# Kernel tuning notes

Hardware: AMD Instinct MI355X
Metric: run time of the kernel (lower is better)

## Reference

```python
import jax, jax.numpy as jnp
import numpy as np

PAST = 16
FUTURE = 4
DIM = 64
INPUT_SIZE = 256
NUM_LAYERS = 3
DILATION = [1, 2, 4, 8]
INPUT_LENGTH = 1024
BATCH = 16
NEG_INF = -1e9


def _dilated_masks(length, num_layers, dilation):
    # mask[i, t, s] == True means position t may NOT attend to position s in layer i.
    # Layer i attends to s = t - k*dilation[i] for k in [0, window) with
    # window = dilation[i+1] // dilation[i] (causal, dilated local window).
    idx = np.arange(length)
    diff = idx[:, None] - idx[None, :]  # t - s
    masks = []
    for i in range(num_layers):
        d = dilation[i]
        window = dilation[i + 1] // d
        allowed = (diff >= 0) & (diff % d == 0) & (diff < window * d)
        masks.append(~allowed)
    return jnp.asarray(np.stack(masks, 0))


def setup_inputs() -> dict:
    key = jax.random.key(0)
    k_inp, k_w, k_b = jax.random.split(key, 3)
    inp = jax.random.normal(k_inp, (BATCH, INPUT_LENGTH, INPUT_SIZE), dtype=jnp.float32)
    # BottleLinear(input_size, output_size): plain Linear over last dim
    out_size = FUTURE * DIM
    bound = 1.0 / np.sqrt(INPUT_SIZE)
    W_out = jax.random.uniform(k_w, (out_size, INPUT_SIZE), minval=-bound, maxval=bound, dtype=jnp.float32)
    b_out = jax.random.uniform(k_b, (out_size,), minval=-bound, maxval=bound, dtype=jnp.float32)
    masks = _dilated_masks(INPUT_LENGTH, NUM_LAYERS, DILATION)
    return {"inp": inp, "W_out": W_out, "b_out": b_out, "masks": masks}


def reference(inp, W_out, b_out, masks):
    # inp: [B, L, D]; masks: [num_layers, L, L] bool (True = masked)
    B, L, D = inp.shape
    scale = 1.0 / jnp.sqrt(jnp.asarray(D, inp.dtype))
    residual = inp[:, PAST:, :DIM][:, :, None, :]  # [B, L-past, 1, dim]
    out = inp
    attns = []
    for i in range(NUM_LAYERS):
        mask = masks[i, :L, :L]
        scores = jnp.einsum('bld,bmd->blm', out, out) * scale
        scores = jnp.where(mask[None], NEG_INF, scores)
        attn = jax.nn.softmax(scores, axis=-1)  # [B, L, L]
        # dropout=0.0 (eval); residual self-attention layer
        out = jnp.einsum('blm,bmd->bld', attn, out) + out
        attns.append(attn)
    o = out[:, PAST:]  # [B, L-past, D]
    o = jnp.einsum('bld,od->blo', o, W_out) + b_out
    o = o.reshape(B, L - PAST, FUTURE, DIM) + residual
    attn_stack = jnp.stack(attns, 1)  # [B, num_layers, L, L]
    return o, attn_stack
```

## Files before the change

### kernel.cpp

```cpp
#include <hip/hip_runtime.h>

#define BATCH 16
#define LEN 1024
#define DIM_IN 256
#define PAST 16
#define OUTROWS (LEN - PAST)
#define NLAYERS 3
#define O_ELEMS ((size_t)BATCH * OUTROWS * 256)

template<int D, int LAYER>
__global__ __launch_bounds__(256) void layer_kernel(const float* __restrict__ in,
                                                    float* __restrict__ out,
                                                    float* __restrict__ attn)
{
    const int w    = threadIdx.x >> 6;
    const int lane = threadIdx.x & 63;
    const int r    = blockIdx.x * 4 + w;
    const int b    = r >> 10;
    const int l    = r & 1023;

    const float4* rowL = (const float4*)(in + (size_t)(b * LEN + l) * DIM_IN);
    float4 x = rowL[lane];
    float4 y = make_float4(0.f, 0.f, 0.f, 0.f);
    if (l >= D) {
        const float4* rowP = (const float4*)(in + (size_t)(b * LEN + l - D) * DIM_IN);
        y = rowP[lane];
    }

    float dot0 = x.x * x.x + x.y * x.y + x.z * x.z + x.w * x.w;
    float dot1 = x.x * y.x + x.y * y.y + x.z * y.z + x.w * y.w;
    #pragma unroll
    for (int off = 32; off; off >>= 1) {
        dot0 += __shfl_xor(dot0, off, 64);
        dot1 += __shfl_xor(dot1, off, 64);
    }

    const float scale = 0.0625f;
    float p0 = 1.f, p1 = 0.f;
    if (l >= D) {
        float s0 = dot0 * scale, s1 = dot1 * scale;
        float m  = fmaxf(s0, s1);
        float e0 = expf(s0 - m), e1 = expf(s1 - m);
        float inv = 1.f / (e0 + e1);
        p0 = e0 * inv;
        p1 = e1 * inv;
    }

    float4* orow = (float4*)(out + (size_t)(b * LEN + l) * DIM_IN);
    const float a0 = 1.f + p0;
    float4 nv;
    nv.x = x.x * a0 + y.x * p1;
    nv.y = x.y * a0 + y.y * p1;
    nv.z = x.z * a0 + y.z * p1;
    nv.w = x.w * a0 + y.w * p1;
    orow[lane] = nv;

    float4* arow = (float4*)(attn + ((size_t)(b * NLAYERS + LAYER) * LEN + l) * (size_t)LEN);
    #pragma unroll
    for (int it = 0; it < 4; ++it) {
        const int col = it * 256 + lane * 4;
        float4 v = make_float4(0.f, 0.f, 0.f, 0.f);
        const int dd = l - col;
        if (dd >= 0 && dd < 4) ((float*)&v)[dd] = p0;
        if (l >= D) {
            const int dp = (l - D) - col;
            if (dp >= 0 && dp < 4) ((float*)&v)[dp] = p1;
        }
        arow[it * 64 + lane] = v;
    }
}

__global__ __launch_bounds__(256) void proj_kernel(const float* __restrict__ outbuf,
                                                   const float* __restrict__ inp,
                                                   const float* __restrict__ W,
                                                   const float* __restrict__ bias,
                                                   float* __restrict__ o)
{
    __shared__ float rows[16][DIM_IN];
    const int bid = blockIdx.x;
    const int b   = bid / 63;
    const int lo0 = (bid % 63) * 16;
    const int t   = threadIdx.x;

    const float4* src = (const float4*)(outbuf + (size_t)(b * LEN + PAST + lo0) * DIM_IN);
    float4* dst = (float4*)rows;
    #pragma unroll
    for (int j = 0; j < 4; ++j) dst[t + 256 * j] = src[t + 256 * j];
    __syncthreads();

    const int c = t;
    float acc[16];
    #pragma unroll
    for (int r2 = 0; r2 < 16; ++r2) acc[r2] = 0.f;

    const float4* W4    = (const float4*)(W + (size_t)c * DIM_IN);
    const float4* rows4 = (const float4*)rows;
    for (int kq = 0; kq < 64; ++kq) {
        float4 wv = W4[kq];
        #pragma unroll
        for (int r2 = 0; r2 < 16; ++r2) {
            float4 xr = rows4[r2 * 64 + kq];
            acc[r2] += wv.x * xr.x + wv.y * xr.y + wv.z * xr.z + wv.w * xr.w;
        }
    }

    const float bv   = bias[c];
    const int   dcol = c & 63;
    #pragma unroll
    for (int r2 = 0; r2 < 16; ++r2) {
        const int lo = lo0 + r2;
        const float res = inp[(size_t)(b * LEN + PAST + lo) * DIM_IN + dcol];
        o[(size_t)(b * OUTROWS + lo) * 256 + c] = acc[r2] + bv + res;
    }
}

extern "C" void kernel_launch(void* const* d_in, const int* in_sizes, int n_in,
                              void* d_out, int out_size, void* d_ws, size_t ws_size,
                              hipStream_t stream) {
    const float* inp   = (const float*)d_in[0];
    const float* W_out = (const float*)d_in[1];
    const float* b_out = (const float*)d_in[2];

    float* o_out     = (float*)d_out;
    float* attn_out  = o_out + O_ELEMS;

    float* buf0 = (float*)d_ws;
    float* buf1 = buf0 + (size_t)BATCH * LEN * DIM_IN;

    const int nblk = BATCH * LEN / 4;
    layer_kernel<1, 0><<<nblk, 256, 0, stream>>>(inp,  buf0, attn_out);
    layer_kernel<2, 1><<<nblk, 256, 0, stream>>>(buf0, buf1, attn_out);
    layer_kernel<4, 2><<<nblk, 256, 0, stream>>>(buf1, buf0, attn_out);

    proj_kernel<<<BATCH * 63, 256, 0, stream>>>(buf0, inp, W_out, b_out, o_out);
}
```

Baseline: 368.3 us.

## Fuse all attention layers and output projection into one tiled kernel with halo

Replaces three per-layer kernels and the projection kernel with one kernel. Each block loads a 32-row tile plus an 8-row halo into shared memory and runs all three dilated two-tap attention layers there, then does the projection from shared memory. This removes the intermediate global round trips and three launches, at the cost of recomputing the halo rows. Attention-map stores become nontemporal to keep the large write stream from polluting cache.

```diff
diff --git a/kernel.cpp b/kernel.cpp
--- a/kernel.cpp
+++ b/kernel.cpp
@@ -2,115 +2,142 @@
 
 #define BATCH 16
 #define LEN 1024
-#define DIM_IN 256
+#define DIN 256
 #define PAST 16
 #define OUTROWS (LEN - PAST)
-#define NLAYERS 3
+#define NL 3
+#define TROWS 32
+#define HALO 8
+#define NR (TROWS + HALO)
 #define O_ELEMS ((size_t)BATCH * OUTROWS * 256)
 
-template<int D, int LAYER>
-__global__ __launch_bounds__(256) void layer_kernel(const float* __restrict__ in,
-                                                    float* __restrict__ out,
-                                                    float* __restrict__ attn)
+typedef float f4_t __attribute__((ext_vector_type(4)));
+
+__device__ __forceinline__ void layer_step(const float (*S)[DIN], float (*D)[DIN],
+                                           const int DD, const int layer,
+                                           const int b, const int l0,
+                                           const int wave, const int lane,
+                                           float* __restrict__ attn)
 {
-    const int w    = threadIdx.x >> 6;
-    const int lane = threadIdx.x & 63;
-    const int r    = blockIdx.x * 4 + w;
-    const int b    = r >> 10;
-    const int l    = r & 1023;
+    #pragma unroll
+    for (int it = 0; it < NR / 8; ++it) {
+        const int row = it * 8 + wave;
+        const int l   = l0 - HALO + row;
+        const int ry  = (row >= DD) ? (row - DD) : 0;
 
-    const float4* rowL = (const float4*)(in + (size_t)(b * LEN + l) * DIM_IN);
-    float4 x = rowL[lane];
-    float4 y = make_float4(0.f, 0.f, 0.f, 0.f);
-    if (l >= D) {
-        const float4* rowP = (const float4*)(in + (size_t)(b * LEN + l - D) * DIM_IN);
-        y = rowP[lane];
-    }
+        const float4 x = ((const float4*)(S[row]))[lane];
+        const float4 y = ((const float4*)(S[ry]))[lane];
 
-    float dot0 = x.x * x.x + x.y * x.y + x.z * x.z + x.w * x.w;
-    float dot1 = x.x * y.x + x.y * y.y + x.z * y.z + x.w * y.w;
-    #pragma unroll
-    for (int off = 32; off; off >>= 1) {
-        dot0 += __shfl_xor(dot0, off, 64);
-        dot1 += __shfl_xor(dot1, off, 64);
-    }
+        float d0 = x.x * x.x + x.y * x.y + x.z * x.z + x.w * x.w;
+        float d1 = x.x * y.x + x.y * y.y + x.z * y.z + x.w * y.w;
+        #pragma unroll
+        for (int off = 32; off; off >>= 1) {
+            d0 += __shfl_xor(d0, off, 64);
+            d1 += __shfl_xor(d1, off, 64);
+        }
 
-    const float scale = 0.0625f;
-    float p0 = 1.f, p1 = 0.f;
-    if (l >= D) {
-        float s0 = dot0 * scale, s1 = dot1 * scale;
-        float m  = fmaxf(s0, s1);
-        float e0 = expf(s0 - m), e1 = expf(s1 - m);
-        float inv = 1.f / (e0 + e1);
-        p0 = e0 * inv;
-        p1 = e1 * inv;
-    }
+        float p0 = 1.f, p1 = 0.f;
+        if (l >= DD) {
+            const float s0 = d0 * 0.0625f, s1 = d1 * 0.0625f;
+            const float m  = fmaxf(s0, s1);
+            const float e0 = expf(s0 - m), e1 = expf(s1 - m);
+            const float inv = 1.f / (e0 + e1);
+            p0 = e0 * inv;
+            p1 = e1 * inv;
+        }
 
-    float4* orow = (float4*)(out + (size_t)(b * LEN + l) * DIM_IN);
-    const float a0 = 1.f + p0;
-    float4 nv;
-    nv.x = x.x * a0 + y.x * p1;
-    nv.y = x.y * a0 + y.y * p1;
-    nv.z = x.z * a0 + y.z * p1;
-    nv.w = x.w * a0 + y.w * p1;
-    orow[lane] = nv;
+        const float a0 = 1.f + p0;
+        float4 nv;
+        nv.x = fmaf(y.x, p1, x.x * a0);
+        nv.y = fmaf(y.y, p1, x.y * a0);
+        nv.z = fmaf(y.z, p1, x.z * a0);
+        nv.w = fmaf(y.w, p1, x.w * a0);
+        ((float4*)(D[row]))[lane] = nv;
 
-    float4* arow = (float4*)(attn + ((size_t)(b * NLAYERS + LAYER) * LEN + l) * (size_t)LEN);
-    #pragma unroll
-    for (int it = 0; it < 4; ++it) {
-        const int col = it * 256 + lane * 4;
-        float4 v = make_float4(0.f, 0.f, 0.f, 0.f);
-        const int dd = l - col;
-        if (dd >= 0 && dd < 4) ((float*)&v)[dd] = p0;
-        if (l >= D) {
-            const int dp = (l - D) - col;
-            if (dp >= 0 && dp < 4) ((float*)&v)[dp] = p1;
+        if (row >= HALO) {
+            float* arow = attn + (((size_t)(b * NL + layer)) * LEN + l) * (size_t)LEN;
+            #pragma unroll
+            for (int j = 0; j < 4; ++j) {
+                const int col = j * 256 + lane * 4;
+                float4 v = make_float4(0.f, 0.f, 0.f, 0.f);
+                const int dd = l - col;
+                if (dd >= 0 && dd < 4) ((float*)&v)[dd] = p0;
+                if (l >= DD) {
+                    const int dp = (l - DD) - col;
+                    if (dp >= 0 && dp < 4) ((float*)&v)[dp] = p1;
+                }
+                __builtin_nontemporal_store(*(const f4_t*)&v,
+                                            (f4_t*)arow + j * 64 + lane);
+            }
         }
-        arow[it * 64 + lane] = v;
     }
 }
 
-__global__ __launch_bounds__(256) void proj_kernel(const float* __restrict__ outbuf,
-                                                   const float* __restrict__ inp,
-                                                   const float* __restrict__ W,
-                                                   const float* __restrict__ bias,
-                                                   float* __restrict__ o)
+__global__ __launch_bounds__(512, 4) void fused_kernel(const float* __restrict__ inp,
+                                                       const float* __restrict__ W,
+                                                       const float* __restrict__ bias,
+                                                       float* __restrict__ o,
+                                                       float* __restrict__ attn)
 {
-    __shared__ float rows[16][DIM_IN];
-    const int bid = blockIdx.x;
-    const int b   = bid / 63;
-    const int lo0 = (bid % 63) * 16;
-    const int t   = threadIdx.x;
+    __shared__ float A[NR][DIN];
+    __shared__ float Bb[NR][DIN];
 
-    const float4* src = (const float4*)(outbuf + (size_t)(b * LEN + PAST + lo0) * DIM_IN);
-    float4* dst = (float4*)rows;
-    #pragma unroll
-    for (int j = 0; j < 4; ++j) dst[t + 256 * j] = src[t + 256 * j];
+    const int blk  = blockIdx.x;
+    const int b    = blk >> 5;
+    const int l0   = (blk & 31) * TROWS;
+    const int t    = threadIdx.x;
+    const int wave = t >> 6;
+    const int lane = t & 63;
+
+    {
+        float4* dst = (float4*)A;
+        const size_t base = (size_t)b * LEN;
+        #pragma unroll
+        for (int i = 0; i < 5; ++i) {
+            const int idx = i * 512 + t;
+            const int row = idx >> 6;
+            int g = l0 - HALO + row; if (g < 0) g = 0;
+            dst[idx] = ((const float4*)(inp + (base + g) * DIN))[idx & 63];
+        }
+    }
     __syncthreads();
 
-    const int c = t;
+    layer_step(A,  Bb, 1, 0, b, l0, wave, lane, attn);
+    __syncthreads();
+    layer_step(Bb, A,  2, 1, b, l0, wave, lane, attn);
+    __syncthreads();
+    layer_step(A,  Bb, 4, 2, b, l0, wave, lane, attn);
+    __syncthreads();
+
+    const int half = t >> 8;
+    const int c    = t & 255;
     float acc[16];
     #pragma unroll
-    for (int r2 = 0; r2 < 16; ++r2) acc[r2] = 0.f;
+    for (int r = 0; r < 16; ++r) acc[r] = 0.f;
 
-    const float4* W4    = (const float4*)(W + (size_t)c * DIM_IN);
-    const float4* rows4 = (const float4*)rows;
+    const float4* W4 = (const float4*)(W + (size_t)c * DIN);
+    const float4* R4 = (const float4*)(Bb[HALO + half * 16]);
     for (int kq = 0; kq < 64; ++kq) {
-        float4 wv = W4[kq];
+        const float4 wv = W4[kq];
         #pragma unroll
-        for (int r2 = 0; r2 < 16; ++r2) {
-            float4 xr = rows4[r2 * 64 + kq];
-            acc[r2] += wv.x * xr.x + wv.y * xr.y + wv.z * xr.z + wv.w * xr.w;
+        for (int r = 0; r < 16; ++r) {
+            const float4 xr = R4[r * 64 + kq];
+            acc[r] = fmaf(wv.x, xr.x, acc[r]);
+            acc[r] = fmaf(wv.y, xr.y, acc[r]);
+            acc[r] = fmaf(wv.z, xr.z, acc[r]);
+            acc[r] = fmaf(wv.w, xr.w, acc[r]);
         }
     }
 
     const float bv   = bias[c];
     const int   dcol = c & 63;
     #pragma unroll
-    for (int r2 = 0; r2 < 16; ++r2) {
-        const int lo = lo0 + r2;
-        const float res = inp[(size_t)(b * LEN + PAST + lo) * DIM_IN + dcol];
-        o[(size_t)(b * OUTROWS + lo) * 256 + c] = acc[r2] + bv + res;
+    for (int r = 0; r < 16; ++r) {
+        const int l = l0 + half * 16 + r;
+        if (l >= PAST) {
+            const float res = inp[((size_t)b * LEN + l) * DIN + dcol];
+            o[((size_t)b * OUTROWS + (l - PAST)) * 256 + c] = acc[r] + bv + res;
+        }
     }
 }
 
@@ -121,16 +148,9 @@
     const float* W_out = (const float*)d_in[1];
     const float* b_out = (const float*)d_in[2];
 
-    float* o_out     = (float*)d_out;
-    float* attn_out  = o_out + O_ELEMS;
+    float* o_out    = (float*)d_out;
+    float* attn_out = o_out + O_ELEMS;
 
-    float* buf0 = (float*)d_ws;
-    float* buf1 = buf0 + (size_t)BATCH * LEN * DIM_IN;
-
-    const int nblk = BATCH * LEN / 4;
-    layer_kernel<1, 0><<<nblk, 256, 0, stream>>>(inp,  buf0, attn_out);
-    layer_kernel<2, 1><<<nblk, 256, 0, stream>>>(buf0, buf1, attn_out);
-    layer_kernel<4, 2><<<nblk, 256, 0, stream>>>(buf1, buf0, attn_out);
-
-    proj_kernel<<<BATCH * 63, 256, 0, stream>>>(buf0, inp, W_out, b_out, o_out);
+    fused_kernel<<<BATCH * (LEN / TROWS), 512, 0, stream>>>(inp, W_out, b_out,
+                                                            o_out, attn_out);
 }
```

Measured after the change: 303.6 us. -17.6%, faster.
